# Kernel optimization log

Hardware: AMD Instinct MI355X
Metric: run time of the kernel (lower is better)

Reference implementation:

```python
import math
import jax, jax.numpy as jnp
import numpy as np

B, S, D, H, DFF, BASE = 2, 2048, 1024, 16, 4096, 10000.0
HD = D // H  # 64


def setup_inputs() -> dict:
    key = jax.random.key(0)
    ks = jax.random.split(key, 16)
    sc = 0.02
    inp = {
        "x": jax.random.normal(ks[0], (B, S, D), jnp.float32),
        "positions": jnp.arange(S, dtype=jnp.int32),
        "wq": jax.random.normal(ks[1], (D, D), jnp.float32) * sc,
        "bq": jnp.zeros((D,), jnp.float32),
        "wk": jax.random.normal(ks[2], (D, D), jnp.float32) * sc,
        "bk": jnp.zeros((D,), jnp.float32),
        "wv": jax.random.normal(ks[3], (D, D), jnp.float32) * sc,
        "bv": jnp.zeros((D,), jnp.float32),
        "wo": jax.random.normal(ks[4], (D, D), jnp.float32) * sc,
        "bo": jnp.zeros((D,), jnp.float32),
        "phase_bias": jax.random.uniform(ks[5], (H, HD), jnp.float32, -2.0 * math.pi, 0.0),
        "w1": jax.random.normal(ks[6], (D, DFF), jnp.float32) * sc,
        "b1": jnp.zeros((DFF,), jnp.float32),
        "w2": jax.random.normal(ks[7], (DFF, D), jnp.float32) * sc,
        "b2": jnp.zeros((D,), jnp.float32),
        "g1": jnp.ones((D,), jnp.float32),
        "be1": jnp.zeros((D,), jnp.float32),
        "g2": jnp.ones((D,), jnp.float32),
        "be2": jnp.zeros((D,), jnp.float32),
    }
    return inp


def _layernorm(x, g, b):
    mu = jnp.mean(x, -1, keepdims=True)
    var = jnp.mean(jnp.square(x - mu), -1, keepdims=True)
    return (x - mu) / jnp.sqrt(var + 1e-5) * g + b


def _block(x, positions, wq, bq, wk, bk, wv, bv, wo, bo, phase_bias,
           w1, b1, w2, b2, g1, be1, g2, be2):
    # projections -> (B, H, S, HD)
    def heads(w, b):
        return (x @ w + b).reshape(B, S, H, HD).transpose(0, 2, 1, 3)
    q, k, v = heads(wq, bq), heads(wk, bk), heads(wv, bv)

    # PoPE: magnitudes via softplus, phases from position*freq (+ clamped bias for k)
    mu_q = jax.nn.softplus(q)
    mu_k = jax.nn.softplus(k)
    freqs = 1.0 / BASE ** (jnp.arange(HD, dtype=jnp.float32) / HD)      # (HD,)
    pos_ph = positions[:, None].astype(jnp.float32) * freqs[None, :]     # (S, HD)
    q_ph = pos_ph[None, None]                                            # (1,1,S,HD)
    cb = jnp.clip(phase_bias, -2.0 * math.pi, 0.0)
    k_ph = pos_ph[None, None] + cb[None, :, None, :]                     # (1,H,S,HD)
    q_p = jnp.concatenate([mu_q * jnp.cos(q_ph), mu_q * jnp.sin(q_ph)], -1)  # (B,H,S,2HD)
    k_p = jnp.concatenate([mu_k * jnp.cos(k_ph), mu_k * jnp.sin(k_ph)], -1)

    # manual attention with causal mask and softmax1
    scale = 1.0 / math.sqrt(2 * HD)
    scores = jnp.einsum("bhqd,bhkd->bhqk", q_p, k_p) * scale
    causal = jnp.triu(jnp.ones((S, S), bool), 1)
    scores = jnp.where(causal, -jnp.inf, scores)
    m = jnp.max(scores, -1, keepdims=True)  # finite: diagonal always unmasked
    e = jnp.exp(scores - m)
    w = e / (jnp.exp(-m) + jnp.sum(e, -1, keepdims=True))
    attn = jnp.einsum("bhqk,bhkd->bhqd", w, v)
    attn = attn.transpose(0, 2, 1, 3).reshape(B, S, D) @ wo + bo

    h = _layernorm(x + attn, g1, be1)
    ff = jax.nn.relu(h @ w1 + b1) @ w2 + b2
    return _layernorm(h + ff, g2, be2)


def reference(x, positions, wq, bq, wk, bk, wv, bv, wo, bo, phase_bias,
              w1, b1, w2, b2, g1, be1, g2, be2):
    return _block(x, positions, wq, bq, wk, bk, wv, bv, wo, bo, phase_bias,
                  w1, b1, w2, b2, g1, be1, g2, be2)
```

## Files before the change

kernel.cpp:

```cpp
#include <hip/hip_runtime.h>
#include <hip/hip_bf16.h>
#include <math.h>

#define NB 2
#define NS 2048
#define ND 1024
#define NH 16
#define NHD 64
#define NDFF 4096

typedef __attribute__((ext_vector_type(4))) float f32x4;
typedef __attribute__((ext_vector_type(8))) short bf16x8;

__device__ __forceinline__ short f2bf(float f) {
  union { float f; unsigned u; } v; v.f = f;
  unsigned r = v.u + 0x7fffu + ((v.u >> 16) & 1u);
  return (short)(r >> 16);
}
__device__ __forceinline__ float bf2f(unsigned short u) {
  union { unsigned u; float f; } v; v.u = ((unsigned)u) << 16; return v.f;
}
__device__ __forceinline__ float softplus_f(float x) {
  return fmaxf(x, 0.f) + log1pf(__expf(-fabsf(x)));
}
__device__ __forceinline__ void gl16(const short* g, short* l) {
  __builtin_amdgcn_global_load_lds(
      (const __attribute__((address_space(1))) void*)g,
      (__attribute__((address_space(3))) void*)l, 16, 0, 0);
}
__device__ __forceinline__ void xcd_map(int& row0, int& col0) {
  const int gx = gridDim.x, gy = gridDim.y;
  const int bid = blockIdx.y * gx + blockIdx.x;
  const int rows_px = gy >> 3;
  const int xcd = bid & 7, l = bid >> 3;
  row0 = (xcd * rows_px + (l % rows_px)) * 128;
  col0 = (l / rows_px) * 128;
}

__global__ __launch_bounds__(256) void k_prep(
    const float* __restrict__ wq, const float* __restrict__ wk,
    const float* __restrict__ wv, const float* __restrict__ wo,
    const float* __restrict__ w1, const float* __restrict__ w2,
    const float* __restrict__ x,
    short* __restrict__ wqT, short* __restrict__ wkT, short* __restrict__ wvT,
    short* __restrict__ woT, short* __restrict__ w1T, short* __restrict__ w2T,
    short* __restrict__ xb) {
  __shared__ float t[64][65];
  const int bid = blockIdx.x;
  if (bid >= 3072) {
    const int i = (bid - 3072) * 256 + threadIdx.x;
    const float4 a = ((const float4*)x)[i * 2];
    const float4 b = ((const float4*)x)[i * 2 + 1];
    short tmp[8] = { f2bf(a.x), f2bf(a.y), f2bf(a.z), f2bf(a.w),
                     f2bf(b.x), f2bf(b.y), f2bf(b.z), f2bf(b.w) };
    *(int4*)&xb[(size_t)i * 8] = *(const int4*)tmp;
    return;
  }
  const float* W; short* Wt; int K, N, local;
  if (bid < 1024) {
    const int wsel = bid >> 8; local = bid & 255;
    W  = wsel == 0 ? wq  : wsel == 1 ? wk  : wsel == 2 ? wv  : wo;
    Wt = wsel == 0 ? wqT : wsel == 1 ? wkT : wsel == 2 ? wvT : woT;
    K = ND; N = ND;
  } else if (bid < 2048) {
    local = bid - 1024; W = w1; Wt = w1T; K = ND; N = NDFF;
  } else {
    local = bid - 2048; W = w2; Wt = w2T; K = NDFF; N = ND;
  }
  const int nx = N >> 6;
  const int n0 = (local % nx) * 64, k0 = (local / nx) * 64;
  for (int i = threadIdx.x; i < 4096; i += 256) {
    const int r = i >> 6, c = i & 63;
    t[r][c] = W[(size_t)(k0 + r) * N + n0 + c];
  }
  __syncthreads();
  for (int i = threadIdx.x; i < 4096; i += 256) {
    const int r = i >> 6, c = i & 63;
    Wt[(size_t)(n0 + r) * K + k0 + c] = f2bf(t[c][r]);
  }
}

__global__ __launch_bounds__(256) void k_pope_pv(const short* __restrict__ qb,
    const short* __restrict__ kb, const short* __restrict__ vb,
    const int* __restrict__ positions, const float* __restrict__ phb,
    short* __restrict__ qp, short* __restrict__ kp, short* __restrict__ vt) {
  __shared__ short t[64][72];
  const int bid = blockIdx.x;
  if (bid < 2048) {
    const size_t i8 = ((size_t)bid * 256 + threadIdx.x) * 8;
    const int d0 = (int)(i8 & 63);
    const int h  = (int)((i8 >> 6) & 15);
    const int s  = (int)((i8 >> 10) & 2047);
    const int b  = (int)(i8 >> 21);
    const float posf = (float)positions[s];
    int4 qv = *(const int4*)&qb[i8];
    int4 kv = *(const int4*)&kb[i8];
    const short* qs = (const short*)&qv;
    const short* ks = (const short*)&kv;
    short qc[8], qsn[8], kc[8], ksn[8];
#pragma unroll
    for (int j = 0; j < 8; j++) {
      const int d = d0 + j;
      const float freq = __expf(-(float)d * (float)(9.210340371976184 / 64.0));
      const float muq = softplus_f(bf2f((unsigned short)qs[j]));
      const float muk = softplus_f(bf2f((unsigned short)ks[j]));
      float cb = phb[h * 64 + d];
      cb = fminf(fmaxf(cb, -6.283185307179586f), 0.f);
      float snq, csq, snk, csk;
      __sincosf(posf * freq, &snq, &csq);
      __sincosf(posf * freq + cb, &snk, &csk);
      qc[j] = f2bf(muq * csq); qsn[j] = f2bf(muq * snq);
      kc[j] = f2bf(muk * csk); ksn[j] = f2bf(muk * snk);
    }
    const size_t o = (((size_t)(b * 16 + h) * NS + s) * 128) + d0;
    *(int4*)&qp[o] = *(const int4*)qc;
    *(int4*)&qp[o + 64] = *(const int4*)qsn;
    *(int4*)&kp[o] = *(const int4*)kc;
    *(int4*)&kp[o + 64] = *(const int4*)ksn;
  } else {
    const int local = bid - 2048;
    const int bh = local >> 5, b = bh >> 4, h = bh & 15;
    const int s0 = (local & 31) * 64;
    for (int i = threadIdx.x; i < 512; i += 256) {
      const int sl = i >> 3, d8 = (i & 7) * 8;
      int4 vv = *(const int4*)&vb[((size_t)(b * NS + s0 + sl) * NH + h) * NHD + d8];
      const short* sp = (const short*)&vv;
#pragma unroll
      for (int j = 0; j < 8; j++) t[d8 + j][sl] = sp[j];
    }
    __syncthreads();
    for (int i = threadIdx.x; i < 512; i += 256) {
      const int d = i >> 3, c8 = (i & 7) * 8;
      *(int4*)&vt[((size_t)bh * 64 + d) * NS + s0 + c8] = *(const int4*)&t[d][c8];
    }
  }
}

#define BKK 32

__device__ __forceinline__ void gemm_core(const short* __restrict__ A,
    const short* __restrict__ Wt, const int K, const int kbeg, const int kend,
    const int row0, const int col0, short* lsA, short* lsB, f32x4 acc[4][4]) {
  const int tid = threadIdx.x;
  const int lane = tid & 63, wave = tid >> 6;
  const int lr = lane & 15, lk8 = (lane >> 4) << 3;
  const int wr = wave >> 1, wc = wave & 1;
  const int srow = lane >> 2, scol = (lane & 3) << 3;
  const int wbase = wave * 32;
#pragma unroll
  for (int m = 0; m < 4; m++)
#pragma unroll
    for (int n = 0; n < 4; n++) acc[m][n] = 0.f;
  const short* gA0 = &A[(size_t)(row0 + wbase + srow) * K + scol];
  const short* gA1 = gA0 + (size_t)16 * K;
  const short* gB0 = &Wt[(size_t)(col0 + wbase + srow) * K + scol];
  const short* gB1 = gB0 + (size_t)16 * K;
  short* const lA0 = lsA + wbase * 32;
  short* const lB0 = lsB + wbase * 32;
  auto stage = [&](int buf, int kk) {
    const int o = buf * 4096;
    gl16(gA0 + kk, lA0 + o);
    gl16(gA1 + kk, lA0 + o + 512);
    gl16(gB0 + kk, lB0 + o);
    gl16(gB1 + kk, lB0 + o + 512);
  };
  stage(0, kbeg);
  __syncthreads();
  int cur = 0;
  for (int k0 = kbeg; k0 < kend; k0 += BKK) {
    if (k0 + BKK < kend) stage(cur ^ 1, k0 + BKK);
    const short* la = lsA + cur * 4096;
    const short* lb = lsB + cur * 4096;
    bf16x8 af[4], bf_[4];
#pragma unroll
    for (int m = 0; m < 4; m++)
      af[m] = *(const bf16x8*)&la[(wr * 64 + m * 16 + lr) * 32 + lk8];
#pragma unroll
    for (int n = 0; n < 4; n++)
      bf_[n] = *(const bf16x8*)&lb[(wc * 64 + n * 16 + lr) * 32 + lk8];
#pragma unroll
    for (int m = 0; m < 4; m++)
#pragma unroll
      for (int n = 0; n < 4; n++)
        acc[m][n] = __builtin_amdgcn_mfma_f32_16x16x32_bf16(af[m], bf_[n], acc[m][n], 0, 0, 0);
    __syncthreads();
    cur ^= 1;
  }
}

template<int RELU, int OUTBF16>
__global__ __launch_bounds__(256) void k_gemm(const short* __restrict__ A,
    const short* __restrict__ Wt, const float* __restrict__ bias,
    void* __restrict__ C, int M, int N, int K) {
  __shared__ short lsA[2 * 4096], lsB[2 * 4096];
  f32x4 acc[4][4];
  int row0, col0;
  xcd_map(row0, col0);
  gemm_core(A, Wt, K, 0, K, row0, col0, lsA, lsB, acc);
  const int lane = threadIdx.x & 63, wave = threadIdx.x >> 6;
  const int lr = lane & 15, r4 = (lane >> 4) << 2;
  const int wr = wave >> 1, wc = wave & 1;
#pragma unroll
  for (int m = 0; m < 4; m++) {
#pragma unroll
    for (int n = 0; n < 4; n++) {
      const int col = col0 + wc * 64 + n * 16 + lr;
      const float bv = bias[col];
#pragma unroll
      for (int r = 0; r < 4; r++) {
        const int row = row0 + wr * 64 + m * 16 + r4 + r;
        float val = acc[m][n][r] + bv;
        if (RELU) val = fmaxf(val, 0.f);
        if (OUTBF16) ((short*)C)[(size_t)row * N + col] = f2bf(val);
        else ((float*)C)[(size_t)row * N + col] = val;
      }
    }
  }
}

__global__ __launch_bounds__(256) void k_gemm3(const short* __restrict__ xb,
    const short* __restrict__ wqT, const short* __restrict__ wkT,
    const short* __restrict__ wvT, const float* __restrict__ bq,
    const float* __restrict__ bk, const float* __restrict__ bv,
    short* __restrict__ qb, short* __restrict__ kb, short* __restrict__ vb) {
  __shared__ short lsA[2 * 4096], lsB[2 * 4096];
  const int z = blockIdx.z;
  const short* Wt = (z == 0) ? wqT : (z == 1) ? wkT : wvT;
  const float* bias = (z == 0) ? bq : (z == 1) ? bk : bv;
  short* C = (z == 0) ? qb : (z == 1) ? kb : vb;
  f32x4 acc[4][4];
  int row0, col0;
  xcd_map(row0, col0);
  gemm_core(xb, Wt, ND, 0, ND, row0, col0, lsA, lsB, acc);
  const int lane = threadIdx.x & 63, wave = threadIdx.x >> 6;
  const int lr = lane & 15, r4 = (lane >> 4) << 2;
  const int wr = wave >> 1, wc = wave & 1;
#pragma unroll
  for (int m = 0; m < 4; m++) {
#pragma unroll
    for (int n = 0; n < 4; n++) {
      const int col = col0 + wc * 64 + n * 16 + lr;
      const float bvs = bias[col];
#pragma unroll
      for (int r = 0; r < 4; r++) {
        const int row = row0 + wr * 64 + m * 16 + r4 + r;
        C[(size_t)row * ND + col] = f2bf(acc[m][n][r] + bvs);
      }
    }
  }
}

__global__ __launch_bounds__(256) void k_gemm_sk(const short* __restrict__ A,
    const short* __restrict__ Wt, float* __restrict__ C0, float* __restrict__ C1,
    int M, int N, int K) {
  __shared__ short lsA[2 * 4096], lsB[2 * 4096];
  f32x4 acc[4][4];
  const int z = blockIdx.z;
  const int khalf = K >> 1, kbeg = z * khalf, kend = kbeg + khalf;
  int row0, col0;
  xcd_map(row0, col0);
  gemm_core(A, Wt, K, kbeg, kend, row0, col0, lsA, lsB, acc);
  float* C = z ? C1 : C0;
  const int lane = threadIdx.x & 63, wave = threadIdx.x >> 6;
  const int lr = lane & 15, r4 = (lane >> 4) << 2;
  const int wr = wave >> 1, wc = wave & 1;
#pragma unroll
  for (int m = 0; m < 4; m++) {
#pragma unroll
    for (int n = 0; n < 4; n++) {
      const int col = col0 + wc * 64 + n * 16 + lr;
#pragma unroll
      for (int r = 0; r < 4; r++) {
        const int row = row0 + wr * 64 + m * 16 + r4 + r;
        C[(size_t)row * N + col] = acc[m][n][r];
      }
    }
  }
}

__device__ __forceinline__ void attn_proc(const bf16x8 aq[4], f32x4 acc_o[4],
    f32x4& accS, const int rowb, const int kb,
    const short (*kpl)[136], const short (*vl)[72], short (*pl)[72],
    const int lr, const int lk) {
  f32x4 s_acc[4];
#pragma unroll
  for (int n = 0; n < 4; n++) s_acc[n] = 0.f;
#pragma unroll
  for (int ks = 0; ks < 4; ks++) {
    bf16x8 bk_[4];
#pragma unroll
    for (int n = 0; n < 4; n++)
      bk_[n] = *(const bf16x8*)&kpl[n * 16 + lr][ks * 32 + lk * 8];
#pragma unroll
    for (int n = 0; n < 4; n++)
      s_acc[n] = __builtin_amdgcn_mfma_f32_16x16x32_bf16(aq[ks], bk_[n], s_acc[n], 0, 0, 0);
  }
  const float scale2 = 0.1275174333f;
  const bool domask = (kb + 63 > rowb);
#pragma unroll
  for (int n = 0; n < 4; n++) {
#pragma unroll
    for (int r = 0; r < 4; r++) {
      float p = exp2f(s_acc[n][r] * scale2);
      if (domask) {
        const int rel = rowb + lk * 4 + r - kb;
        p = (n * 16 + lr <= rel) ? p : 0.f;
      }
      s_acc[n][r] = p;
    }
  }
#pragma unroll
  for (int n = 0; n < 4; n++)
#pragma unroll
    for (int r = 0; r < 4; r++)
      pl[lk * 4 + r][n * 16 + lr] = f2bf(s_acc[n][r]);
  bf16x8 bones;
#pragma unroll
  for (int i = 0; i < 8; i++) bones[i] = (short)0x3F80;
#pragma unroll
  for (int ks = 0; ks < 2; ks++) {
    const bf16x8 ap = *(const bf16x8*)&pl[lr][ks * 32 + lk * 8];
    accS = __builtin_amdgcn_mfma_f32_16x16x32_bf16(ap, bones, accS, 0, 0, 0);
    bf16x8 bv_[4];
#pragma unroll
    for (int nd = 0; nd < 4; nd++)
      bv_[nd] = *(const bf16x8*)&vl[nd * 16 + lr][ks * 32 + lk * 8];
#pragma unroll
    for (int nd = 0; nd < 4; nd++)
      acc_o[nd] = __builtin_amdgcn_mfma_f32_16x16x32_bf16(ap, bv_[nd], acc_o[nd], 0, 0, 0);
  }
}

__global__ __launch_bounds__(512) void k_attn3(
    const short* __restrict__ qp, const short* __restrict__ kp,
    const short* __restrict__ vt, short* __restrict__ attn) {
  __shared__ short kp_l[2][64][136];
  __shared__ short v_l[2][64][72];
  __shared__ short p_l[8][16][72];
  const int bh = blockIdx.y, b = bh >> 4, h = bh & 15;
  const int bx = blockIdx.x;
  const int tid = threadIdx.x, wave = tid >> 6, lane = tid & 63;
  const int lr = lane & 15, lk = lane >> 4;
  const int tHeavy = 31 - bx;
  const int myTile = (wave < 4) ? tHeavy : bx;
  const int rowb = myTile * 64 + (wave & 3) * 16;
  const int nch = tHeavy + 1;

  bf16x8 aq[4];
  {
    const short* qrow = qp + ((size_t)bh * NS + rowb + lr) * 128;
#pragma unroll
    for (int ks = 0; ks < 4; ks++)
      aq[ks] = *(const bf16x8*)&qrow[ks * 32 + lk * 8];
  }
  f32x4 acc[4], accS;
  accS = 0.f;
#pragma unroll
  for (int n = 0; n < 4; n++) acc[n] = 0.f;

  const short* kpb = kp + (size_t)bh * NS * 128;
  const short* vtb = vt + (size_t)bh * 64 * NS;
  const int krow = tid >> 3, kcol = (tid & 7) * 16;
  const int vrow = tid >> 3, vcol = (tid & 7) * 8;

  int4 rk0, rk1, rv;
  {
    const short* s = &kpb[(size_t)krow * 128 + kcol];
    rk0 = ((const int4*)s)[0]; rk1 = ((const int4*)s)[1];
    rv = *(const int4*)&vtb[(size_t)vrow * NS + vcol];
  }
  ((int4*)&kp_l[0][krow][kcol])[0] = rk0;
  ((int4*)&kp_l[0][krow][kcol])[1] = rk1;
  *(int4*)&v_l[0][vrow][vcol] = rv;
  __syncthreads();

  for (int c = 0; c < nch; c++) {
    const int kb = c * 64;
    const int cur = c & 1;
    const bool more = (c + 1) < nch;
    if (more) {
      const int kb2 = kb + 64;
      const short* s = &kpb[(size_t)(kb2 + krow) * 128 + kcol];
      rk0 = ((const int4*)s)[0]; rk1 = ((const int4*)s)[1];
      rv = *(const int4*)&vtb[(size_t)vrow * NS + kb2 + vcol];
    }
    if (rowb + 15 >= kb)
      attn_proc(aq, acc, accS, rowb, kb, kp_l[cur], v_l[cur], p_l[wave], lr, lk);
    if (more) {
      ((int4*)&kp_l[cur ^ 1][krow][kcol])[0] = rk0;
      ((int4*)&kp_l[cur ^ 1][krow][kcol])[1] = rk1;
      *(int4*)&v_l[cur ^ 1][vrow][vcol] = rv;
    }
    __syncthreads();
  }
  float inv[4];
#pragma unroll
  for (int r = 0; r < 4; r++) inv[r] = 1.f / (1.f + accS[r]);
#pragma unroll
  for (int nd = 0; nd < 4; nd++) {
#pragma unroll
    for (int r = 0; r < 4; r++) {
      const int d = nd * 16 + lr;
      const int row = rowb + lk * 4 + r;
      attn[(((size_t)b * NS + row) * NH + h) * NHD + d] = f2bf(acc[nd][r] * inv[r]);
    }
  }
}

template<int RBF16, int OUTBF16>
__global__ __launch_bounds__(256) void k_ln3(const float* __restrict__ A0,
    const float* __restrict__ A1, const float* __restrict__ badd,
    const void* __restrict__ Rv, const float* __restrict__ g,
    const float* __restrict__ be, void* __restrict__ out) {
  const int row = blockIdx.x, tid = threadIdx.x;
  const float4 a0 = ((const float4*)(A0 + (size_t)row * ND))[tid];
  const float4 a1 = ((const float4*)(A1 + (size_t)row * ND))[tid];
  const float4 bd = ((const float4*)badd)[tid];
  float r0, r1, r2, r3;
  if (RBF16) {
    short4 rr = *(const short4*)((const short*)Rv + (size_t)row * ND + tid * 4);
    r0 = bf2f((unsigned short)rr.x); r1 = bf2f((unsigned short)rr.y);
    r2 = bf2f((unsigned short)rr.z); r3 = bf2f((unsigned short)rr.w);
  } else {
    const float4 rr = ((const float4*)((const float*)Rv + (size_t)row * ND))[tid];
    r0 = rr.x; r1 = rr.y; r2 = rr.z; r3 = rr.w;
  }
  const float x0 = a0.x + a1.x + bd.x + r0;
  const float x1 = a0.y + a1.y + bd.y + r1;
  const float x2 = a0.z + a1.z + bd.z + r2;
  const float x3 = a0.w + a1.w + bd.w + r3;
  float s = x0 + x1 + x2 + x3;
  float sq = x0 * x0 + x1 * x1 + x2 * x2 + x3 * x3;
#pragma unroll
  for (int off = 32; off; off >>= 1) {
    s += __shfl_xor(s, off);
    sq += __shfl_xor(sq, off);
  }
  __shared__ float ss[4], ssq[4];
  const int wave = tid >> 6, lane = tid & 63;
  if (lane == 0) { ss[wave] = s; ssq[wave] = sq; }
  __syncthreads();
  s = ss[0] + ss[1] + ss[2] + ss[3];
  sq = ssq[0] + ssq[1] + ssq[2] + ssq[3];
  const float mu = s * (1.f / (float)ND);
  const float var = sq * (1.f / (float)ND) - mu * mu;
  const float rstd = rsqrtf(var + 1e-5f);
  const float4 gg = ((const float4*)g)[tid];
  const float4 bb = ((const float4*)be)[tid];
  const float o0 = (x0 - mu) * rstd * gg.x + bb.x;
  const float o1 = (x1 - mu) * rstd * gg.y + bb.y;
  const float o2 = (x2 - mu) * rstd * gg.z + bb.z;
  const float o3 = (x3 - mu) * rstd * gg.w + bb.w;
  if (OUTBF16) {
    short4 ov = { f2bf(o0), f2bf(o1), f2bf(o2), f2bf(o3) };
    *(short4*)((short*)out + (size_t)row * ND + tid * 4) = ov;
  } else {
    float4 ov = { o0, o1, o2, o3 };
    ((float4*)((float*)out + (size_t)row * ND))[tid] = ov;
  }
}

extern "C" void kernel_launch(void* const* d_in, const int* in_sizes, int n_in,
                              void* d_out, int out_size, void* d_ws, size_t ws_size,
                              hipStream_t stream) {
  const float* x   = (const float*)d_in[0];
  const int*   pos = (const int*)d_in[1];
  const float* wq  = (const float*)d_in[2];
  const float* bq  = (const float*)d_in[3];
  const float* wk  = (const float*)d_in[4];
  const float* bk  = (const float*)d_in[5];
  const float* wv  = (const float*)d_in[6];
  const float* bv  = (const float*)d_in[7];
  const float* wo  = (const float*)d_in[8];
  const float* bo  = (const float*)d_in[9];
  const float* phb = (const float*)d_in[10];
  const float* w1  = (const float*)d_in[11];
  const float* b1  = (const float*)d_in[12];
  const float* w2  = (const float*)d_in[13];
  const float* b2  = (const float*)d_in[14];
  const float* g1  = (const float*)d_in[15];
  const float* be1 = (const float*)d_in[16];
  const float* g2  = (const float*)d_in[17];
  const float* be2 = (const float*)d_in[18];

  char* ws = (char*)d_ws;
  const size_t MB = 1024 * 1024;
  if (ws_size < 112 * MB) return;
  short* qb     = (short*)(ws + 0 * MB);
  short* kb     = (short*)(ws + 8 * MB);
  short* vb     = (short*)(ws + 16 * MB);
  short* qp     = (short*)(ws + 24 * MB);
  short* kp     = (short*)(ws + 40 * MB);
  short* vt     = (short*)(ws + 56 * MB);
  short* xb     = (short*)(ws + 64 * MB);
  short* attnb  = (short*)(ws + 72 * MB);
  float* attnC0 = (float*)(ws + 0 * MB);
  float* attnC1 = (float*)(ws + 24 * MB);
  short* hb     = (short*)(ws + 16 * MB);
  short* ffh    = (short*)(ws + 40 * MB);
  float* ffC0   = (float*)(ws + 72 * MB);
  float* ffC1   = (float*)(ws + 0 * MB);
  short* wqT    = (short*)(ws + 88 * MB);
  short* wkT    = (short*)(ws + 90 * MB);
  short* wvT    = (short*)(ws + 92 * MB);
  short* woT    = (short*)(ws + 94 * MB);
  short* w1T    = (short*)(ws + 96 * MB);
  short* w2T    = (short*)(ws + 104 * MB);

  dim3 blk(256);
  k_prep<<<dim3(5120), blk, 0, stream>>>(wq, wk, wv, wo, w1, w2, x,
                                         wqT, wkT, wvT, woT, w1T, w2T, xb);
  k_gemm3<<<dim3(ND / 128, (NB * NS) / 128, 3), blk, 0, stream>>>(
      xb, wqT, wkT, wvT, bq, bk, bv, qb, kb, vb);
  k_pope_pv<<<dim3(3072), blk, 0, stream>>>(qb, kb, vb, pos, phb, qp, kp, vt);
  k_attn3<<<dim3(16, NB * NH), dim3(512), 0, stream>>>(qp, kp, vt, attnb);
  k_gemm_sk<<<dim3(ND / 128, (NB * NS) / 128, 2), blk, 0, stream>>>(
      attnb, woT, attnC0, attnC1, NB * NS, ND, ND);
  k_ln3<0, 1><<<dim3(NB * NS), blk, 0, stream>>>(attnC0, attnC1, bo, x, g1, be1, hb);
  k_gemm<1, 1><<<dim3(NDFF / 128, (NB * NS) / 128), blk, 0, stream>>>(
      hb, w1T, b1, ffh, NB * NS, NDFF, ND);
  k_gemm_sk<<<dim3(ND / 128, (NB * NS) / 128, 2), blk, 0, stream>>>(
      ffh, w2T, ffC0, ffC1, NB * NS, ND, NDFF);
  k_ln3<1, 0><<<dim3(NB * NS), blk, 0, stream>>>(ffC0, ffC1, b2, hb, g2, be2, (float*)d_out);
}
```

Before: 275.6 us.

## Fold softmax scale into Q, sum probabilities in registers, remap attention blocks per XCD

Folds the score scale (log2e/sqrt(128)) into the Q magnitudes in the PoPE kernel, so the attention inner loop calls the raw exp2 builtin with no multiply. The row-sum is now built by accumulating truncated-to-bf16 probabilities in registers and reducing across lanes with shuffles at the end, replacing the extra MFMA against a ones vector. Block indices are remapped so that blocks sharing a batch-head land on the same XCD, aiming for better L2 reuse of K/V. Probabilities are truncated rather than rounded to bf16, a small change in numerics.

```diff
diff --git a/kernel.cpp b/kernel.cpp
--- a/kernel.cpp
+++ b/kernel.cpp
@@ -93,6 +93,7 @@
     const int s  = (int)((i8 >> 10) & 2047);
     const int b  = (int)(i8 >> 21);
     const float posf = (float)positions[s];
+    const float QSC = 0.12751743305610407f;
     int4 qv = *(const int4*)&qb[i8];
     int4 kv = *(const int4*)&kb[i8];
     const short* qs = (const short*)&qv;
@@ -102,7 +103,7 @@
     for (int j = 0; j < 8; j++) {
       const int d = d0 + j;
       const float freq = __expf(-(float)d * (float)(9.210340371976184 / 64.0));
-      const float muq = softplus_f(bf2f((unsigned short)qs[j]));
+      const float muq = softplus_f(bf2f((unsigned short)qs[j])) * QSC;
       const float muk = softplus_f(bf2f((unsigned short)ks[j]));
       float cb = phb[h * 64 + d];
       cb = fminf(fmaxf(cb, -6.283185307179586f), 0.f);
@@ -279,7 +280,7 @@
 }
 
 __device__ __forceinline__ void attn_proc(const bf16x8 aq[4], f32x4 acc_o[4],
-    f32x4& accS, const int rowb, const int kb,
+    float l_p[4], const int rowb, const int kb,
     const short (*kpl)[136], const short (*vl)[72], short (*pl)[72],
     const int lr, const int lk) {
   f32x4 s_acc[4];
@@ -295,32 +296,24 @@
     for (int n = 0; n < 4; n++)
       s_acc[n] = __builtin_amdgcn_mfma_f32_16x16x32_bf16(aq[ks], bk_[n], s_acc[n], 0, 0, 0);
   }
-  const float scale2 = 0.1275174333f;
   const bool domask = (kb + 63 > rowb);
 #pragma unroll
   for (int n = 0; n < 4; n++) {
 #pragma unroll
     for (int r = 0; r < 4; r++) {
-      float p = exp2f(s_acc[n][r] * scale2);
+      float p = __builtin_amdgcn_exp2f(s_acc[n][r]);
       if (domask) {
         const int rel = rowb + lk * 4 + r - kb;
         p = (n * 16 + lr <= rel) ? p : 0.f;
       }
-      s_acc[n][r] = p;
-    }
-  }
-#pragma unroll
-  for (int n = 0; n < 4; n++)
-#pragma unroll
-    for (int r = 0; r < 4; r++)
-      pl[lk * 4 + r][n * 16 + lr] = f2bf(s_acc[n][r]);
-  bf16x8 bones;
-#pragma unroll
-  for (int i = 0; i < 8; i++) bones[i] = (short)0x3F80;
+      unsigned pu = __float_as_uint(p) & 0xFFFF0000u;
+      l_p[r] += __uint_as_float(pu);
+      pl[lk * 4 + r][n * 16 + lr] = (short)(pu >> 16);
+    }
+  }
 #pragma unroll
   for (int ks = 0; ks < 2; ks++) {
     const bf16x8 ap = *(const bf16x8*)&pl[lr][ks * 32 + lk * 8];
-    accS = __builtin_amdgcn_mfma_f32_16x16x32_bf16(ap, bones, accS, 0, 0, 0);
     bf16x8 bv_[4];
 #pragma unroll
     for (int nd = 0; nd < 4; nd++)
@@ -337,8 +330,11 @@
   __shared__ short kp_l[2][64][136];
   __shared__ short v_l[2][64][72];
   __shared__ short p_l[8][16][72];
-  const int bh = blockIdx.y, b = bh >> 4, h = bh & 15;
-  const int bx = blockIdx.x;
+  const int bid = blockIdx.y * gridDim.x + blockIdx.x;
+  const int xcd = bid & 7, o = bid >> 3;
+  const int bh = xcd * 4 + (o >> 4);
+  const int bx = o & 15;
+  const int b = bh >> 4, h = bh & 15;
   const int tid = threadIdx.x, wave = tid >> 6, lane = tid & 63;
   const int lr = lane & 15, lk = lane >> 4;
   const int tHeavy = 31 - bx;
@@ -353,8 +349,10 @@
     for (int ks = 0; ks < 4; ks++)
       aq[ks] = *(const bf16x8*)&qrow[ks * 32 + lk * 8];
   }
-  f32x4 acc[4], accS;
-  accS = 0.f;
+  f32x4 acc[4];
+  float lsum[4];
+#pragma unroll
+  for (int r = 0; r < 4; r++) lsum[r] = 0.f;
 #pragma unroll
   for (int n = 0; n < 4; n++) acc[n] = 0.f;
 
@@ -385,7 +383,7 @@
       rv = *(const int4*)&vtb[(size_t)vrow * NS + kb2 + vcol];
     }
     if (rowb + 15 >= kb)
-      attn_proc(aq, acc, accS, rowb, kb, kp_l[cur], v_l[cur], p_l[wave], lr, lk);
+      attn_proc(aq, acc, lsum, rowb, kb, kp_l[cur], v_l[cur], p_l[wave], lr, lk);
     if (more) {
       ((int4*)&kp_l[cur ^ 1][krow][kcol])[0] = rk0;
       ((int4*)&kp_l[cur ^ 1][krow][kcol])[1] = rk1;
@@ -393,16 +391,20 @@
     }
     __syncthreads();
   }
-  float inv[4];
-#pragma unroll
-  for (int r = 0; r < 4; r++) inv[r] = 1.f / (1.f + accS[r]);
+#pragma unroll
+  for (int r = 0; r < 4; r++) {
+    float s = lsum[r];
+#pragma unroll
+    for (int off = 8; off; off >>= 1) s += __shfl_xor(s, off);
+    lsum[r] = 1.f / (1.f + s);
+  }
 #pragma unroll
   for (int nd = 0; nd < 4; nd++) {
 #pragma unroll
     for (int r = 0; r < 4; r++) {
       const int d = nd * 16 + lr;
       const int row = rowb + lk * 4 + r;
-      attn[(((size_t)b * NS + row) * NH + h) * NHD + d] = f2bf(acc[nd][r] * inv[r]);
+      attn[(((size_t)b * NS + row) * NH + h) * NHD + d] = f2bf(acc[nd][r] * lsum[r]);
     }
   }
 }
```

Result: faster. 265.7 us (median of 3 runs) (-3.6%).
